# Performance work log

Hardware: AMD Instinct MI355X
Metric: run time of the kernel (lower is better)

Reference implementation:

```python
import jax, jax.numpy as jnp
import numpy as np

jax.config.update("jax_enable_x64", True)

B, N, M_EQ, D_INEQ = 64, 128, 32, 64
RHO = 1.0
THRES = 1e-5
MAX_ITERS = 5000  # safety cap (original loops until relative objective change <= 1e-5)


def setup_inputs() -> dict:
    key = jax.random.key(0)
    kL, kq, kG, kA, kx0, ks = jax.random.split(key, 6)
    L = jax.random.normal(kL, (B, N, N))
    Q = jnp.einsum('bij,bkj->bik', L, L) / N + jnp.eye(N)  # SPD, well-conditioned
    q = jax.random.normal(kq, (B, N))
    G = jax.random.normal(kG, (B, D_INEQ, N))
    A = jax.random.normal(kA, (B, M_EQ, N))
    x0 = jax.random.normal(kx0, (B, N))
    slack = jax.random.uniform(ks, (B, D_INEQ)) + 0.1
    h = jnp.einsum('bdn,bn->bd', G, x0) + slack  # strictly feasible ineq
    b = jnp.einsum('bmn,bn->bm', A, x0)          # feasible eq
    f32 = jnp.float32
    return {"Q": Q.astype(f32), "q": q.astype(f32), "G": G.astype(f32),
            "h": h.astype(f32), "A": A.astype(f32), "b": b.astype(f32)}


def _alt_diff_batch(Q, q, G, h, A, b):
    """Batched Alt-Diff ADMM QP solve; returns (x [B,n], dx/dq [B,n,n])."""
    Bb, n = q.shape
    d = h.shape[1]
    m = b.shape[1]
    dt = Q.dtype
    AtA = jnp.einsum('bmi,bmj->bij', A, A)
    GtG = jnp.einsum('bdi,bdj->bij', G, G)
    R = -jnp.linalg.inv(Q + RHO * AtA + RHO * GtG)
    ATb = RHO * jnp.einsum('bmn,bm->bn', A, b)
    GTh = RHO * jnp.einsum('bdn,bd->bn', G, h)
    eye = jnp.eye(n, dtype=dt)

    def obj(x):
        return 0.5 * jnp.einsum('bi,bij,bj->b', x, Q, x) + jnp.einsum('bi,bi->b', q, x)

    init = dict(
        xk=jnp.zeros((Bb, n), dt), sk=jnp.zeros((Bb, d), dt),
        lamb=jnp.zeros((Bb, m), dt), nu=jnp.zeros((Bb, d), dt),
        dxk=jnp.zeros((Bb, n, n), dt), dsk=jnp.zeros((Bb, d, n), dt),
        dlamb=jnp.zeros((Bb, m, n), dt), dnu=jnp.zeros((Bb, d, n), dt),
        res_prev=jnp.full((Bb,), 1000.0, dt),   # res = [1000, -100] init
        res_cur=jnp.full((Bb,), -100.0, dt),
        done=jnp.zeros((Bb,), bool),
        it=jnp.zeros((), jnp.int32),
    )

    def cond(s):
        return jnp.logical_and(jnp.any(~s["done"]), s["it"] < MAX_ITERS)

    def body(s):
        xk = jnp.einsum('bij,bj->bi', R,
                        q + jnp.einsum('bmn,bm->bn', A, s["lamb"])
                          + jnp.einsum('bdn,bd->bn', G, s["nu"]) - ATb
                          + RHO * jnp.einsum('bdn,bd->bn', G, s["sk"]) - GTh)
        dxk = jnp.einsum('bij,bjk->bik', R,
                         eye + jnp.einsum('bmn,bmk->bnk', A, s["dlamb"])
                             + jnp.einsum('bdn,bdk->bnk', G, s["dnu"])
                             + RHO * jnp.einsum('bdn,bdk->bnk', G, s["dsk"]))
        Gx = jnp.einsum('bdn,bn->bd', G, xk)
        sk = jax.nn.relu(-(1.0 / RHO) * s["nu"] - (Gx - h))
        sgn = (sk > 0).astype(dt)  # sgn applied to already-relu'd sk, as in source
        dsk = (-1.0 / RHO) * sgn[:, :, None] * (s["dnu"] + RHO * jnp.einsum('bdn,bnk->bdk', G, dxk))
        lamb = s["lamb"] + RHO * (jnp.einsum('bmn,bn->bm', A, xk) - b)
        dlamb = s["dlamb"] + RHO * jnp.einsum('bmn,bnk->bmk', A, dxk)
        nu = s["nu"] + RHO * (Gx + sk - h)
        dnu = s["dnu"] + RHO * (jnp.einsum('bdn,bnk->bdk', G, dxk) + dsk)
        res_new = obj(xk)

        keep = s["done"]

        def sel(old, new):
            mask = keep.reshape((-1,) + (1,) * (new.ndim - 1))
            return jnp.where(mask, old, new)

        res_prev = jnp.where(keep, s["res_prev"], s["res_cur"])
        res_cur = jnp.where(keep, s["res_cur"], res_new)
        done = keep | (jnp.abs((res_cur - res_prev) / res_prev) <= THRES)
        return dict(
            xk=sel(s["xk"], xk), sk=sel(s["sk"], sk),
            lamb=sel(s["lamb"], lamb), nu=sel(s["nu"], nu),
            dxk=sel(s["dxk"], dxk), dsk=sel(s["dsk"], dsk),
            dlamb=sel(s["dlamb"], dlamb), dnu=sel(s["dnu"], dnu),
            res_prev=res_prev, res_cur=res_cur, done=done, it=s["it"] + 1,
        )

    final = jax.lax.while_loop(cond, body, init)
    return final["xk"], final["dxk"]


def reference(Q, q, G, h, A, b):
    out_dtype = q.dtype
    f64 = jnp.float64
    x, _dx = _alt_diff_batch(Q.astype(f64), q.astype(f64), G.astype(f64),
                             h.astype(f64), A.astype(f64), b.astype(f64))
    return x.astype(out_dtype)
```

## Files before the change

### kernel.cpp

```cpp
#include <hip/hip_runtime.h>

#define NN 128
#define ME 32
#define DI 64
#define NZ 96
#define ROWD 130
#define MAXIT 5000

#define OFF_UN 16640
#define ROWB  (OFF_UN)
#define COLB  (OFF_UN + 256)
#define FPLO_F (2*(OFF_UN))
#define FPHI_F (2*(OFF_UN) + 512)
#define TV0L  (OFF_UN + 384)
#define TV0H  (OFF_UN + 512)
#define TV1   (OFF_UN + 576)
#define FLG   (OFF_UN + 608)
#define YBUF  (OFF_UN)
#define KBUF  (OFF_UN + 1536)
#define CPART (OFF_UN + 1024)
#define VP    (OFF_UN + 1280)
#define BASEV (OFF_UN + 1792)
#define QBV   (OFF_UN + 1888)
#define FPART (OFF_UN + 1024)
#define RHSV  (OFF_UN + 1280)
#define XPART (OFF_UN + 1408)
#define CB    (OFF_UN + 2688)
#define QBUF  (OFF_UN + 2816)
#define V1    (OFF_UN + 2944)
#define V2    (OFF_UN + 3072)
#define HB    (OFF_UN + 3200)
#define BB    (OFF_UN + 3264)
#define CST   (OFF_UN + 3296)
#define ZBF   (OFF_UN + 3304)
#define LDS_DBL (OFF_UN + 3400)

typedef __attribute__((ext_vector_type(2))) float f32x2;

__device__ __forceinline__ float rlf(float v, int lane) {
  return __uint_as_float((unsigned)__builtin_amdgcn_readlane((int)__float_as_uint(v), lane));
}
__device__ __forceinline__ f32x2 fma2(f32x2 a, f32x2 b, f32x2 c) {
  return __builtin_elementwise_fma(a, b, c);
}

#define CPYRANGE(LBASE, KBASE, CNT)                                        \
  _Pragma("unroll") for (int j = 0; j < (CNT); ++j) {                      \
    const int lj = (LBASE) + j, kc = (KBASE) + j;                          \
    float va = (float)ldsd[KBUF + kc*NZ + l];                              \
    float vb = (float)ldsd[KBUF + kc*NZ + 64 + lm];                        \
    if ((lj & 1) == 0) { Kp[lj>>1].x = va; Kp2[lj>>1].x = vb; }            \
    else               { Kp[lj>>1].y = va; Kp2[lj>>1].y = vb; }            \
  }

#define MV2(PA, ZS, L0) {                                                  \
    f32x2 z0 = { rlf(ZS, L0), rlf(ZS, (L0)+1) };                           \
    A0 = fma2(Kp[PA], z0, A0); B0 = fma2(Kp2[PA], z0, B0);                 \
    f32x2 z1 = { rlf(ZS, (L0)+2), rlf(ZS, (L0)+3) };                       \
    A1 = fma2(Kp[(PA)+1], z1, A1); B1 = fma2(Kp2[(PA)+1], z1, B1); }
#define MV1(PA, ZS, L0) {                                                  \
    f32x2 z0 = { rlf(ZS, L0), rlf(ZS, (L0)+1) };                           \
    A0 = fma2(Kp[PA], z0, A0); B0 = fma2(Kp2[PA], z0, B0); }

__global__ __launch_bounds__(256, 1) void altdiff_kernel(
    const float* __restrict__ Qg, const float* __restrict__ qg,
    const float* __restrict__ Gg, const float* __restrict__ hg,
    const float* __restrict__ Ag, const float* __restrict__ bg,
    float* __restrict__ out)
{
  extern __shared__ double ldsd[];
  float* const ldsf = (float*)ldsd;

  const int bidx = blockIdx.x;
  const int tid  = threadIdx.x;
  const int w    = tid >> 6;
  const int l    = tid & 63;
  const int lm   = l & 31;
  const int ia   = tid & 127;
  const int hh   = tid >> 7;

  const float* Qb = Qg + (size_t)bidx * NN * NN;
  const float* Ab = Ag + (size_t)bidx * ME * NN;
  const float* Gb = Gg + (size_t)bidx * DI * NN;
  const float* qb = qg + (size_t)bidx * NN;
  const float* hb = hg + (size_t)bidx * DI;
  const float* bv = bg + (size_t)bidx * ME;

  if (tid < DI) ldsd[HB + tid] = (double)hb[tid];
  else if (tid < DI + ME) ldsd[BB + tid - DI] = (double)bv[tid - DI];
  if (tid >= 128) ldsd[QBUF + tid - 128] = (double)qb[tid - 128];

  const int r = tid >> 4, c = tid & 15;
  double acc[8][8];

  {
    const float4* Q4 = (const float4*)Qb;
#pragma unroll
    for (int rr = 0; rr < 8; ++rr) {
      float4 q0 = Q4[((8*r+rr) << 5) + 2*c];
      float4 q1 = Q4[((8*r+rr) << 5) + 2*c + 1];
      acc[rr][0]=(double)q0.x; acc[rr][1]=(double)q0.y; acc[rr][2]=(double)q0.z; acc[rr][3]=(double)q0.w;
      acc[rr][4]=(double)q1.x; acc[rr][5]=(double)q1.y; acc[rr][6]=(double)q1.z; acc[rr][7]=(double)q1.w;
    }
    const float4* A4 = (const float4*)Ab;
    for (int m = 0; m < ME; ++m) {
      float4 u0 = A4[(m << 5) + 2*r], u1 = A4[(m << 5) + 2*r + 1];
      float4 v0 = A4[(m << 5) + 2*c], v1 = A4[(m << 5) + 2*c + 1];
      double uu[8] = {(double)u0.x,(double)u0.y,(double)u0.z,(double)u0.w,
                      (double)u1.x,(double)u1.y,(double)u1.z,(double)u1.w};
      double vv[8] = {(double)v0.x,(double)v0.y,(double)v0.z,(double)v0.w,
                      (double)v1.x,(double)v1.y,(double)v1.z,(double)v1.w};
#pragma unroll
      for (int rr = 0; rr < 8; ++rr)
#pragma unroll
        for (int cc = 0; cc < 8; ++cc)
          acc[rr][cc] = fma(uu[rr], vv[cc], acc[rr][cc]);
    }
    const float4* G4 = (const float4*)Gb;
    for (int d = 0; d < DI; ++d) {
      float4 u0 = G4[(d << 5) + 2*r], u1 = G4[(d << 5) + 2*r + 1];
      float4 v0 = G4[(d << 5) + 2*c], v1 = G4[(d << 5) + 2*c + 1];
      double uu[8] = {(double)u0.x,(double)u0.y,(double)u0.z,(double)u0.w,
                      (double)u1.x,(double)u1.y,(double)u1.z,(double)u1.w};
      double vv[8] = {(double)v0.x,(double)v0.y,(double)v0.z,(double)v0.w,
                      (double)v1.x,(double)v1.y,(double)v1.z,(double)v1.w};
#pragma unroll
      for (int rr = 0; rr < 8; ++rr)
#pragma unroll
        for (int cc = 0; cc < 8; ++cc)
          acc[rr][cc] = fma(uu[rr], vv[cc], acc[rr][cc]);
    }
  }

  {
    if (r == 0) {
#pragma unroll
      for (int cc = 0; cc < 8; ++cc) ldsd[ROWB + 8*c + cc] = acc[0][cc];
    }
    if (c == 0) {
#pragma unroll
      for (int rr = 0; rr < 8; ++rr) ldsd[COLB + 8*r + rr] = acc[rr][0];
    }
    __syncthreads();
    for (int k = 0; k < NN; ++k) {
      const int pb = (k & 1) << 7;
      const int krt = k >> 3, kcl = k & 7;
      double rowk[8], colv[8];
#pragma unroll
      for (int cc = 0; cc < 8; ++cc) rowk[cc] = ldsd[ROWB + pb + 8*c + cc];
#pragma unroll
      for (int rr = 0; rr < 8; ++rr) colv[rr] = ldsd[COLB + pb + 8*r + rr];
      const double dkk  = ldsd[ROWB + pb + k];
      const double rcpd = 1.0 / dkk;
      double rdv[8];
#pragma unroll
      for (int cc = 0; cc < 8; ++cc) rdv[cc] = rowk[cc] * rcpd;
      const bool pivR = (r == krt), pivC = (c == krt);
#pragma unroll
      for (int rr = 0; rr < 8; ++rr) {
        const double cv = colv[rr] * rcpd;
        const bool pr = pivR && (rr == kcl);
#pragma unroll
        for (int cc = 0; cc < 8; ++cc) {
          double gen = fma(-cv, rowk[cc], acc[rr][cc]);
          acc[rr][cc] = pr ? rdv[cc] : gen;
        }
      }
      if (pivC) {
#pragma unroll
        for (int cc = 0; cc < 8; ++cc) if (cc == kcl) {
#pragma unroll
          for (int rr = 0; rr < 8; ++rr) {
            const bool pr2 = pivR && (rr == kcl);
            acc[rr][cc] = pr2 ? -rcpd : colv[rr] * rcpd;
          }
        }
      }
      if (k < NN - 1) {
        const int pb2 = ((k + 1) & 1) << 7;
        const int krt2 = (k + 1) >> 3, kcl2 = (k + 1) & 7;
        if (r == krt2) {
#pragma unroll
          for (int rr = 0; rr < 8; ++rr) if (rr == kcl2) {
#pragma unroll
            for (int cc = 0; cc < 8; ++cc) ldsd[ROWB + pb2 + 8*c + cc] = acc[rr][cc];
          }
        }
        if (c == krt2) {
#pragma unroll
          for (int cc = 0; cc < 8; ++cc) if (cc == kcl2) {
#pragma unroll
            for (int rr = 0; rr < 8; ++rr) ldsd[COLB + pb2 + 8*r + rr] = acc[rr][cc];
          }
        }
      }
      __syncthreads();
    }
#pragma unroll
    for (int rr = 0; rr < 8; ++rr) {
      double2* dst = (double2*)(ldsd + (8*r+rr)*ROWD + 8*c);
#pragma unroll
      for (int t = 0; t < 4; ++t) dst[t] = make_double2(acc[rr][2*t], acc[rr][2*t+1]);
    }
  }
  __syncthreads();

  f32x2 Kp[15], Kp2[15];
  for (int blk = 0; blk < 8; ++blk) {
    {
      const float* gp[6];
#pragma unroll
      for (int jj = 0; jj < 6; ++jj) {
        int it = 12*blk + 6*hh + jj;
        gp[jj] = (it < DI) ? (Gb + it*NN) : (Ab + (it - DI)*NN);
      }
      double a2[6] = {0,0,0,0,0,0};
#pragma unroll 4
      for (int t = 0; t < NN; ++t) {
        double rv = ldsd[t*ROWD + ia];
#pragma unroll
        for (int jj = 0; jj < 6; ++jj)
          a2[jj] = fma(rv, (double)gp[jj][t], a2[jj]);
      }
      double2* yst = (double2*)(ldsd + YBUF + ia*12 + 6*hh);
#pragma unroll
      for (int p = 0; p < 3; ++p) yst[p] = make_double2(a2[2*p], a2[2*p+1]);
    }
    __syncthreads();
    {
      const int r2 = (ia < NZ) ? ia : 0;
      const float* brow = (r2 < DI) ? (Gb + r2*NN) : (Ab + (r2 - DI)*NN);
      double a2[6] = {0,0,0,0,0,0};
#pragma unroll 4
      for (int t = 0; t < NN; ++t) {
        double bvv = (double)brow[t];
        const double2* yr = (const double2*)(ldsd + YBUF + t*12 + 6*hh);
        double2 y0 = yr[0], y1 = yr[1], y2 = yr[2];
        a2[0] = fma(bvv, y0.x, a2[0]); a2[1] = fma(bvv, y0.y, a2[1]);
        a2[2] = fma(bvv, y1.x, a2[2]); a2[3] = fma(bvv, y1.y, a2[3]);
        a2[4] = fma(bvv, y2.x, a2[4]); a2[5] = fma(bvv, y2.y, a2[5]);
      }
      if (ia < NZ) {
#pragma unroll
        for (int jj = 0; jj < 6; ++jj) ldsd[KBUF + (6*hh + jj)*NZ + ia] = a2[jj];
      }
    }
    __syncthreads();
    if (w == 0) {
      if (blk == 0)      { CPYRANGE(0,  0, 12) }
      else if (blk == 1) { CPYRANGE(12, 0, 12) }
    } else if (w == 1) {
      if (blk == 2)      { CPYRANGE(0,  0, 12) }
      else if (blk == 3) { CPYRANGE(12, 0, 4) }
    } else if (w == 2) {
      if (blk == 3)      { CPYRANGE(0,  4, 8) }
      else if (blk == 4) { CPYRANGE(8,  0, 12) }
      else if (blk == 5) { CPYRANGE(20, 0, 10) }
    } else {
      if (blk == 5)      { CPYRANGE(0,  10, 2) }
      else if (blk == 6) { CPYRANGE(2,  0, 12) }
      else if (blk == 7) { CPYRANGE(14, 0, 12) }
    }
    __syncthreads();
  }

  {
    double s = 0;
#pragma unroll 8
    for (int jc = 0; jc < 48; ++jc) {
      int j = 48*hh + jc;
      double coef = (j < DI) ? ldsd[HB + j] : ldsd[BB + j - DI];
      const float* src = (j < DI) ? (Gb + j*NN) : (Ab + (j - DI)*NN);
      s = fma(-(double)src[ia], coef, s);
    }
    ldsd[CPART + hh*128 + ia] = s;
  }
  __syncthreads();
  if (tid < NN) ldsd[CB + tid] = ldsd[QBUF + tid] + ldsd[CPART + tid] + ldsd[CPART + 128 + tid];
  __syncthreads();

  {
    double a = 0, b2 = 0;
#pragma unroll 4
    for (int tt = 0; tt < 64; ++tt) {
      int t = 64*hh + tt;
      double rv = ldsd[t*ROWD + ia];
      a  = fma(rv, ldsd[CB + t], a);
      b2 = fma(rv, ldsd[QBUF + t], b2);
    }
    ldsd[VP + hh*128 + ia] = a;
    ldsd[VP + 256 + hh*128 + ia] = b2;
  }
  __syncthreads();
  if (tid < NN) {
    ldsd[V1 + tid] = ldsd[VP + tid] + ldsd[VP + 128 + tid];
    ldsd[V2 + tid] = ldsd[VP + 256 + tid] + ldsd[VP + 384 + tid];
  }
  __syncthreads();

  {
    const int r2 = (ia < NZ) ? ia : 0;
    const float* brow = (r2 < DI) ? (Gb + r2*NN) : (Ab + (r2 - DI)*NN);
    const int voff = hh ? V2 : V1;
    double s = 0;
#pragma unroll 4
    for (int t = 0; t < NN; ++t) s = fma((double)brow[t], ldsd[voff + t], s);
    if (ia < NZ) ldsd[(hh ? QBV : BASEV) + ia] = s;
  }
  if (w == 0) {
    double pc = ldsd[V1+l]*ldsd[CB+l]   + ldsd[V1+64+l]*ldsd[CB+64+l];
    double pq = ldsd[V1+l]*ldsd[QBUF+l] + ldsd[V1+64+l]*ldsd[QBUF+64+l];
#pragma unroll
    for (int off = 32; off >= 1; off >>= 1) { pc += __shfl_xor(pc, off); pq += __shfl_xor(pq, off); }
    if (l == 0) { ldsd[CST] = pc; ldsd[CST+1] = pq; }
  }
  __syncthreads();

  const double baseA = ldsd[BASEV + l];
  const double baseB = ldsd[BASEV + 64 + lm];
  const double qvA   = ldsd[QBV + l];
  const double qvB   = ldsd[QBV + 64 + lm];
  const double hb2   = ldsd[HB + l] - baseA;
  const double bb2   = baseB - ldsd[BB + lm];
  const double S_uc  = ldsd[CST], S_qu = ldsd[CST + 1];
  double hnb = hb2, lb = bb2;
  double zlo = 0.0, zhi = 0.0;
  double zAlo = 0.0, zAhi = 0.0, zBlo = 0.0, zBhi = 0.0, zClo = 0.0, zChi = 0.0;
  double res_prev = 1000.0, res_cur = -100.0;

  {
    ldsf[FPLO_F + (w << 6) + l] = 0.f;
    if (l < 32) ldsf[FPHI_F + (w << 5) + l] = 0.f;
    if (tid == 0) { ldsd[FLG] = 0.0; ldsd[FLG + 1] = 0.0; }
  }

  for (int it = 0; it < MAXIT + 3; ++it) {
    __syncthreads();
    const int buf = it & 1, nbuf = buf ^ 1;
    const int bprev = (it + 1) & 1;
    double fl = ldsd[FLG + bprev];
    float p0 = 0.f, p1 = 0.f, p2 = 0.f, p3 = 0.f, q0 = 0.f, q1 = 0.f, q2 = 0.f, q3 = 0.f;
    if (w != 3) {
      const int fb = FPLO_F + (buf << 8) + l;
      p0 = ldsf[fb]; p1 = ldsf[fb + 64]; p2 = ldsf[fb + 128]; p3 = ldsf[fb + 192];
    }
    if (w >= 2) {
      const int fb = FPHI_F + (buf << 7) + lm;
      q0 = ldsf[fb]; q1 = ldsf[fb + 32]; q2 = ldsf[fb + 64]; q3 = ldsf[fb + 96];
    }
    double t1v[16];
    if (w == 1) {
      const double2* tp = (const double2*)(ldsd + TV1 + bprev*16);
#pragma unroll
      for (int u = 0; u < 8; ++u) { double2 v = tp[u]; t1v[2*u] = v.x; t1v[2*u+1] = v.y; }
    }
    double a40 = 0, a41 = 0, a42 = 0, a43 = 0, a44 = 0, a45 = 0;
    if (w == 3) {
      const int g = l & 15;
      const double* tl = ldsd + TV0L + bprev*64;
      const double* th = ldsd + TV0H + bprev*32;
      a40 = tl[g]; a41 = tl[g + 16]; a42 = tl[g + 32]; a43 = tl[g + 48];
      a44 = th[g]; a45 = th[g + 16];
    }
    double slo = 0.0, t = 0.0, shi = 0.0, lamn = 0.0;
    float zflo = 0.f, zfhi = 0.f;
    if (w != 3) {
      float s = (p0 + p1) + (p2 + p3);
      slo = (double)s; t = hnb - slo;
      zflo = (float)fabs(t);
    }
    if (w >= 2) {
      float sh = (q0 + q1) + (q2 + q3);
      shi = (double)sh; lamn = lb + shi;
      zfhi = (float)lamn;
    }
    if (it >= 3 && fl != 0.0) break;
    if (w == 0) { zClo = zBlo; zBlo = zAlo; zAlo = zlo; }
    if (w == 3) { zChi = zBhi; zBhi = zAhi; zAhi = zhi; }
    if (it < MAXIT) {
      if (w == 0) zlo = fabs(t);
      if (w != 3) hnb = hb2 + fmin(t, 0.0);
      if (w == 3) zhi = lamn;
      if (w >= 2) lb = lamn + bb2;
      f32x2 A0 = {0.f, 0.f}, A1 = A0, B0 = A0, B1 = A0;
      if (w == 0) {
        MV2(0, zflo, 0)  MV2(2, zflo, 4)  MV2(4, zflo, 8)
        MV2(6, zflo, 12) MV2(8, zflo, 16) MV2(10, zflo, 20)
      } else if (w == 1) {
        MV2(0, zflo, 24) MV2(2, zflo, 28) MV2(4, zflo, 32) MV2(6, zflo, 36)
      } else if (w == 2) {
        MV2(0, zflo, 40) MV2(2, zflo, 44) MV2(4, zflo, 48)
        MV2(6, zflo, 52) MV2(8, zflo, 56) MV2(10, zflo, 60)
        MV2(12, zfhi, 0) MV1(14, zfhi, 4)
      } else {
        MV2(0, zfhi, 6)  MV2(2, zfhi, 10) MV2(4, zfhi, 14)
        MV2(6, zfhi, 18) MV2(8, zfhi, 22) MV2(10, zfhi, 26)
        MV1(12, zfhi, 30)
      }
      f32x2 As = A0 + A1, Bs = B0 + B1;
      float pa0 = As.x + As.y;
      float pa1 = Bs.x + Bs.y;
      ldsf[FPLO_F + (nbuf << 8) + (w << 6) + l] = pa0;
      if (l < 32) ldsf[FPHI_F + (nbuf << 7) + (w << 5) + l] = pa1;
      if (w == 0) {
        double yfull = slo + baseA;
        double tvl = fma(qvA, zAlo, -0.5*(zAlo*(baseA + yfull) + yfull*yfull));
        ldsd[TV0L + buf*64 + l] = tvl;
      }
      if (w == 3) {
        double yfB = shi + baseB;
        double tvh = fma(qvB, zAhi, -0.5*(zAhi*(baseB + yfB) + yfB*yfB));
        if (l < 32) ldsd[TV0H + buf*32 + l] = tvh;
      }
    }
    if (w == 3 && l < 16 && it >= 1 && it <= MAXIT)
      ldsd[TV1 + buf*16 + l] = ((a40 + a41) + (a42 + a43)) + (a44 + a45);
    if (w == 1 && it >= 2 && it <= MAXIT + 1) {
      double s1 = ((t1v[0] + t1v[1]) + (t1v[2] + t1v[3])) + ((t1v[4] + t1v[5]) + (t1v[6] + t1v[7]));
      double s2 = ((t1v[8] + t1v[9]) + (t1v[10] + t1v[11])) + ((t1v[12] + t1v[13]) + (t1v[14] + t1v[15]));
      double obj = (s1 + s2) - 0.5*S_uc + S_qu;
      res_prev = res_cur; res_cur = obj;
      if (l == 0)
        ldsd[FLG + buf] = (fabs(res_cur - res_prev) <= 1e-5 * fabs(res_prev)) ? 1.0 : 0.0;
    }
  }

  if (w == 0) ldsd[ZBF + l] = zClo;
  if (w == 3 && l < 32) ldsd[ZBF + 64 + l] = zChi;
  __syncthreads();
  {
    double s = 0;
#pragma unroll 8
    for (int jc = 0; jc < 48; ++jc) {
      int j = 48*hh + jc;
      double zj = ldsd[ZBF + j];
      const float* src = (j < DI) ? (Gb + j*NN) : (Ab + (j - DI)*NN);
      s = fma((double)src[ia], zj, s);
    }
    ldsd[FPART + hh*128 + ia] = s;
  }
  __syncthreads();
  if (tid < NN) ldsd[RHSV + tid] = ldsd[CB + tid] + ldsd[FPART + tid] + ldsd[FPART + 128 + tid];
  __syncthreads();
  {
    double s = 0;
#pragma unroll 4
    for (int tt = 0; tt < 64; ++tt) {
      int t = 64*hh + tt;
      s = fma(ldsd[t*ROWD + ia], ldsd[RHSV + t], s);
    }
    ldsd[XPART + hh*128 + ia] = s;
  }
  __syncthreads();
  if (tid < NN)
    out[(size_t)bidx * NN + tid] = (float)(ldsd[XPART + tid] + ldsd[XPART + 128 + tid]);
}

extern "C" void kernel_launch(void* const* d_in, const int* in_sizes, int n_in,
                              void* d_out, int out_size, void* d_ws, size_t ws_size,
                              hipStream_t stream) {
  (void)in_sizes; (void)n_in; (void)out_size; (void)d_ws; (void)ws_size;
  const float* Q = (const float*)d_in[0];
  const float* q = (const float*)d_in[1];
  const float* G = (const float*)d_in[2];
  const float* h = (const float*)d_in[3];
  const float* A = (const float*)d_in[4];
  const float* b = (const float*)d_in[5];
  float* out = (float*)d_out;
  const size_t lds_bytes = (size_t)LDS_DBL * sizeof(double);
  altdiff_kernel<<<dim3(64), dim3(256), lds_bytes, stream>>>(Q, q, G, h, A, b, out);
}
```

Before: 686.0 us.

## Add fifth wavefront for objective tracking and rebalance ADMM matvec across four waves

Launches 320 threads per block. A dedicated fifth wavefront handles objective evaluation, the reduction and the convergence flag, so the four compute waves only run the per-iteration matvec and the projection/dual updates. The K rows are redistributed so each of the four waves owns exactly 24 columns, and the partial-sum buffers are packed as float2. The objective terms now go through LDS exchange buffers, and the prologue/epilogue phases are guarded with tid<256, which adds some sync and occupancy cost.

```diff
diff --git a/kernel.cpp b/kernel.cpp
--- a/kernel.cpp
+++ b/kernel.cpp
@@ -10,12 +10,12 @@
 #define OFF_UN 16640
 #define ROWB  (OFF_UN)
 #define COLB  (OFF_UN + 256)
-#define FPLO_F (2*(OFF_UN))
-#define FPHI_F (2*(OFF_UN) + 512)
-#define TV0L  (OFF_UN + 384)
-#define TV0H  (OFF_UN + 512)
-#define TV1   (OFF_UN + 576)
-#define FLG   (OFF_UN + 608)
+#define PPK   (OFF_UN)
+#define ZEXL  (OFF_UN + 512)
+#define ZEXH  (OFF_UN + 640)
+#define TVX   (OFF_UN + 704)
+#define TV16  (OFF_UN + 832)
+#define FLG   (OFF_UN + 864)
 #define YBUF  (OFF_UN)
 #define KBUF  (OFF_UN + 1536)
 #define CPART (OFF_UN + 1024)
@@ -44,32 +44,19 @@
   return __builtin_elementwise_fma(a, b, c);
 }
 
-#define CPYRANGE(LBASE, KBASE, CNT)                                        \
-  _Pragma("unroll") for (int j = 0; j < (CNT); ++j) {                      \
-    const int lj = (LBASE) + j, kc = (KBASE) + j;                          \
-    float va = (float)ldsd[KBUF + kc*NZ + l];                              \
-    float vb = (float)ldsd[KBUF + kc*NZ + 64 + lm];                        \
-    if ((lj & 1) == 0) { Kp[lj>>1].x = va; Kp2[lj>>1].x = vb; }            \
-    else               { Kp[lj>>1].y = va; Kp2[lj>>1].y = vb; }            \
-  }
-
 #define MV2(PA, ZS, L0) {                                                  \
     f32x2 z0 = { rlf(ZS, L0), rlf(ZS, (L0)+1) };                           \
     A0 = fma2(Kp[PA], z0, A0); B0 = fma2(Kp2[PA], z0, B0);                 \
     f32x2 z1 = { rlf(ZS, (L0)+2), rlf(ZS, (L0)+3) };                       \
     A1 = fma2(Kp[(PA)+1], z1, A1); B1 = fma2(Kp2[(PA)+1], z1, B1); }
-#define MV1(PA, ZS, L0) {                                                  \
-    f32x2 z0 = { rlf(ZS, L0), rlf(ZS, (L0)+1) };                           \
-    A0 = fma2(Kp[PA], z0, A0); B0 = fma2(Kp2[PA], z0, B0); }
-
-__global__ __launch_bounds__(256, 1) void altdiff_kernel(
+
+__global__ __launch_bounds__(320, 1) void altdiff_kernel(
     const float* __restrict__ Qg, const float* __restrict__ qg,
     const float* __restrict__ Gg, const float* __restrict__ hg,
     const float* __restrict__ Ag, const float* __restrict__ bg,
     float* __restrict__ out)
 {
   extern __shared__ double ldsd[];
-  float* const ldsf = (float*)ldsd;
 
   const int bidx = blockIdx.x;
   const int tid  = threadIdx.x;
@@ -88,12 +75,12 @@
 
   if (tid < DI) ldsd[HB + tid] = (double)hb[tid];
   else if (tid < DI + ME) ldsd[BB + tid - DI] = (double)bv[tid - DI];
-  if (tid >= 128) ldsd[QBUF + tid - 128] = (double)qb[tid - 128];
+  if (tid >= 128 && tid < 256) ldsd[QBUF + tid - 128] = (double)qb[tid - 128];
 
   const int r = tid >> 4, c = tid & 15;
   double acc[8][8];
 
-  {
+  if (tid < 256) {
     const float4* Q4 = (const float4*)Qb;
 #pragma unroll
     for (int rr = 0; rr < 8; ++rr) {
@@ -132,7 +119,7 @@
     }
   }
 
-  {
+  if (tid < 256) {
     if (r == 0) {
 #pragma unroll
       for (int cc = 0; cc < 8; ++cc) ldsd[ROWB + 8*c + cc] = acc[0][cc];
@@ -141,8 +128,10 @@
 #pragma unroll
       for (int rr = 0; rr < 8; ++rr) ldsd[COLB + 8*r + rr] = acc[rr][0];
     }
-    __syncthreads();
-    for (int k = 0; k < NN; ++k) {
+  }
+  __syncthreads();
+  for (int k = 0; k < NN; ++k) {
+    if (tid < 256) {
       const int pb = (k & 1) << 7;
       const int krt = k >> 3, kcl = k & 7;
       double rowk[8], colv[8];
@@ -194,8 +183,10 @@
           }
         }
       }
-      __syncthreads();
-    }
+    }
+    __syncthreads();
+  }
+  if (tid < 256) {
 #pragma unroll
     for (int rr = 0; rr < 8; ++rr) {
       double2* dst = (double2*)(ldsd + (8*r+rr)*ROWD + 8*c);
@@ -205,9 +196,9 @@
   }
   __syncthreads();
 
-  f32x2 Kp[15], Kp2[15];
+  f32x2 Kp[12], Kp2[12];
   for (int blk = 0; blk < 8; ++blk) {
-    {
+    if (tid < 256) {
       const float* gp[6];
 #pragma unroll
       for (int jj = 0; jj < 6; ++jj) {
@@ -227,7 +218,7 @@
       for (int p = 0; p < 3; ++p) yst[p] = make_double2(a2[2*p], a2[2*p+1]);
     }
     __syncthreads();
-    {
+    if (tid < 256) {
       const int r2 = (ia < NZ) ? ia : 0;
       const float* brow = (r2 < DI) ? (Gb + r2*NN) : (Ab + (r2 - DI)*NN);
       double a2[6] = {0,0,0,0,0,0};
@@ -246,25 +237,29 @@
       }
     }
     __syncthreads();
-    if (w == 0) {
-      if (blk == 0)      { CPYRANGE(0,  0, 12) }
-      else if (blk == 1) { CPYRANGE(12, 0, 12) }
-    } else if (w == 1) {
-      if (blk == 2)      { CPYRANGE(0,  0, 12) }
-      else if (blk == 3) { CPYRANGE(12, 0, 4) }
-    } else if (w == 2) {
-      if (blk == 3)      { CPYRANGE(0,  4, 8) }
-      else if (blk == 4) { CPYRANGE(8,  0, 12) }
-      else if (blk == 5) { CPYRANGE(20, 0, 10) }
-    } else {
-      if (blk == 5)      { CPYRANGE(0,  10, 2) }
-      else if (blk == 6) { CPYRANGE(2,  0, 12) }
-      else if (blk == 7) { CPYRANGE(14, 0, 12) }
+    if (w == (blk >> 1)) {
+      if ((blk & 1) == 0) {
+#pragma unroll
+        for (int p = 0; p < 6; ++p) {
+          Kp [p].x = (float)ldsd[KBUF + (2*p  )*NZ + l];
+          Kp [p].y = (float)ldsd[KBUF + (2*p+1)*NZ + l];
+          Kp2[p].x = (float)ldsd[KBUF + (2*p  )*NZ + 64 + lm];
+          Kp2[p].y = (float)ldsd[KBUF + (2*p+1)*NZ + 64 + lm];
+        }
+      } else {
+#pragma unroll
+        for (int p = 0; p < 6; ++p) {
+          Kp [6+p].x = (float)ldsd[KBUF + (2*p  )*NZ + l];
+          Kp [6+p].y = (float)ldsd[KBUF + (2*p+1)*NZ + l];
+          Kp2[6+p].x = (float)ldsd[KBUF + (2*p  )*NZ + 64 + lm];
+          Kp2[6+p].y = (float)ldsd[KBUF + (2*p+1)*NZ + 64 + lm];
+        }
+      }
     }
     __syncthreads();
   }
 
-  {
+  if (tid < 256) {
     double s = 0;
 #pragma unroll 8
     for (int jc = 0; jc < 48; ++jc) {
@@ -279,7 +274,7 @@
   if (tid < NN) ldsd[CB + tid] = ldsd[QBUF + tid] + ldsd[CPART + tid] + ldsd[CPART + 128 + tid];
   __syncthreads();
 
-  {
+  if (tid < 256) {
     double a = 0, b2 = 0;
 #pragma unroll 4
     for (int tt = 0; tt < 64; ++tt) {
@@ -298,7 +293,7 @@
   }
   __syncthreads();
 
-  {
+  if (tid < 256) {
     const int r2 = (ia < NZ) ? ia : 0;
     const float* brow = (r2 < DI) ? (Gb + r2*NN) : (Ab + (r2 - DI)*NN);
     const int voff = hh ? V2 : V1;
@@ -329,106 +324,98 @@
   double res_prev = 1000.0, res_cur = -100.0;
 
   {
-    ldsf[FPLO_F + (w << 6) + l] = 0.f;
-    if (l < 32) ldsf[FPHI_F + (w << 5) + l] = 0.f;
+    if (w < 4) ((float2*)&ldsd[PPK + (w << 6) + l])[0] = make_float2(0.f, 0.f);
+    if (w == 0) ldsd[ZEXL + 64 + l] = 0.0;
+    if (w == 3 && l < 32) ldsd[ZEXH + 32 + l] = 0.0;
     if (tid == 0) { ldsd[FLG] = 0.0; ldsd[FLG + 1] = 0.0; }
   }
 
   for (int it = 0; it < MAXIT + 3; ++it) {
     __syncthreads();
     const int buf = it & 1, nbuf = buf ^ 1;
-    const int bprev = (it + 1) & 1;
-    double fl = ldsd[FLG + bprev];
-    float p0 = 0.f, p1 = 0.f, p2 = 0.f, p3 = 0.f, q0 = 0.f, q1 = 0.f, q2 = 0.f, q3 = 0.f;
-    if (w != 3) {
-      const int fb = FPLO_F + (buf << 8) + l;
-      p0 = ldsf[fb]; p1 = ldsf[fb + 64]; p2 = ldsf[fb + 128]; p3 = ldsf[fb + 192];
-    }
-    if (w >= 2) {
-      const int fb = FPHI_F + (buf << 7) + lm;
-      q0 = ldsf[fb]; q1 = ldsf[fb + 32]; q2 = ldsf[fb + 64]; q3 = ldsf[fb + 96];
-    }
-    double t1v[16];
-    if (w == 1) {
-      const double2* tp = (const double2*)(ldsd + TV1 + bprev*16);
-#pragma unroll
-      for (int u = 0; u < 8; ++u) { double2 v = tp[u]; t1v[2*u] = v.x; t1v[2*u+1] = v.y; }
-    }
-    double a40 = 0, a41 = 0, a42 = 0, a43 = 0, a44 = 0, a45 = 0;
-    if (w == 3) {
+    const int bprev = nbuf;
+    const double fl = ldsd[FLG + bprev];
+
+    if (w < 4) {
+      const float2* pb = (const float2*)(ldsd + PPK + buf*256);
+      float2 v0 = pb[l], v1 = pb[64 + l], v2 = pb[128 + l], v3 = pb[192 + l];
+      double t = 0.0, lamn = 0.0;
+      float zflo = 0.f, zfhi = 0.f;
+      if (w != 3) {
+        float s = (v0.x + v1.x) + (v2.x + v3.x);
+        t = hnb - (double)s;
+        zflo = (float)fabs(t);
+      }
+      if (w >= 2) {
+        float sh = (v0.y + v1.y) + (v2.y + v3.y);
+        lamn = lb + (double)sh;
+        zfhi = (float)lamn;
+      }
+      if (it >= 3 && fl != 0.0) break;
+      if (w == 0) { zClo = zBlo; zBlo = zAlo; zAlo = zlo; }
+      if (w == 3) { zChi = zBhi; zBhi = zAhi; zAhi = zhi; }
+      if (it < MAXIT) {
+        if (w == 0) { zlo = fabs(t); ldsd[ZEXL + buf*64 + l] = zlo; }
+        if (w != 3) hnb = hb2 + fmin(t, 0.0);
+        if (w == 3) { zhi = lamn; if (l < 32) ldsd[ZEXH + buf*32 + l] = lamn; }
+        if (w >= 2) lb = lamn + bb2;
+        f32x2 A0 = {0.f, 0.f}, A1 = A0, B0 = A0, B1 = A0;
+        if (w == 0) {
+          MV2(0, zflo, 0)  MV2(2, zflo, 4)  MV2(4, zflo, 8)
+          MV2(6, zflo, 12) MV2(8, zflo, 16) MV2(10, zflo, 20)
+        } else if (w == 1) {
+          MV2(0, zflo, 24) MV2(2, zflo, 28) MV2(4, zflo, 32)
+          MV2(6, zflo, 36) MV2(8, zflo, 40) MV2(10, zflo, 44)
+        } else if (w == 2) {
+          MV2(0, zflo, 48) MV2(2, zflo, 52) MV2(4, zflo, 56) MV2(6, zflo, 60)
+          MV2(8, zfhi, 0)  MV2(10, zfhi, 4)
+        } else {
+          MV2(0, zfhi, 8)  MV2(2, zfhi, 12) MV2(4, zfhi, 16)
+          MV2(6, zfhi, 20) MV2(8, zfhi, 24) MV2(10, zfhi, 28)
+        }
+        f32x2 As = A0 + A1, Bs = B0 + B1;
+        ((float2*)&ldsd[PPK + nbuf*256 + (w << 6) + l])[0] =
+            make_float2(As.x + As.y, Bs.x + Bs.y);
+      }
+    } else {
+      const float2* pb = (const float2*)(ldsd + PPK + buf*256);
+      float2 v0 = pb[l], v1 = pb[64 + l], v2 = pb[128 + l], v3 = pb[192 + l];
+      const double zAl = ldsd[ZEXL + bprev*64 + l];
+      const double zAh = ldsd[ZEXH + bprev*32 + lm];
       const int g = l & 15;
-      const double* tl = ldsd + TV0L + bprev*64;
-      const double* th = ldsd + TV0H + bprev*32;
-      a40 = tl[g]; a41 = tl[g + 16]; a42 = tl[g + 32]; a43 = tl[g + 48];
-      a44 = th[g]; a45 = th[g + 16];
-    }
-    double slo = 0.0, t = 0.0, shi = 0.0, lamn = 0.0;
-    float zflo = 0.f, zfhi = 0.f;
-    if (w != 3) {
-      float s = (p0 + p1) + (p2 + p3);
-      slo = (double)s; t = hnb - slo;
-      zflo = (float)fabs(t);
-    }
-    if (w >= 2) {
-      float sh = (q0 + q1) + (q2 + q3);
-      shi = (double)sh; lamn = lb + shi;
-      zfhi = (float)lamn;
-    }
-    if (it >= 3 && fl != 0.0) break;
-    if (w == 0) { zClo = zBlo; zBlo = zAlo; zAlo = zlo; }
-    if (w == 3) { zChi = zBhi; zBhi = zAhi; zAhi = zhi; }
-    if (it < MAXIT) {
-      if (w == 0) zlo = fabs(t);
-      if (w != 3) hnb = hb2 + fmin(t, 0.0);
-      if (w == 3) zhi = lamn;
-      if (w >= 2) lb = lamn + bb2;
-      f32x2 A0 = {0.f, 0.f}, A1 = A0, B0 = A0, B1 = A0;
-      if (w == 0) {
-        MV2(0, zflo, 0)  MV2(2, zflo, 4)  MV2(4, zflo, 8)
-        MV2(6, zflo, 12) MV2(8, zflo, 16) MV2(10, zflo, 20)
-      } else if (w == 1) {
-        MV2(0, zflo, 24) MV2(2, zflo, 28) MV2(4, zflo, 32) MV2(6, zflo, 36)
-      } else if (w == 2) {
-        MV2(0, zflo, 40) MV2(2, zflo, 44) MV2(4, zflo, 48)
-        MV2(6, zflo, 52) MV2(8, zflo, 56) MV2(10, zflo, 60)
-        MV2(12, zfhi, 0) MV1(14, zfhi, 4)
-      } else {
-        MV2(0, zfhi, 6)  MV2(2, zfhi, 10) MV2(4, zfhi, 14)
-        MV2(6, zfhi, 18) MV2(8, zfhi, 22) MV2(10, zfhi, 26)
-        MV1(12, zfhi, 30)
-      }
-      f32x2 As = A0 + A1, Bs = B0 + B1;
-      float pa0 = As.x + As.y;
-      float pa1 = Bs.x + Bs.y;
-      ldsf[FPLO_F + (nbuf << 8) + (w << 6) + l] = pa0;
-      if (l < 32) ldsf[FPHI_F + (nbuf << 7) + (w << 5) + l] = pa1;
-      if (w == 0) {
-        double yfull = slo + baseA;
-        double tvl = fma(qvA, zAlo, -0.5*(zAlo*(baseA + yfull) + yfull*yfull));
-        ldsd[TV0L + buf*64 + l] = tvl;
-      }
-      if (w == 3) {
-        double yfB = shi + baseB;
-        double tvh = fma(qvB, zAhi, -0.5*(zAhi*(baseB + yfB) + yfB*yfB));
-        if (l < 32) ldsd[TV0H + buf*32 + l] = tvh;
-      }
-    }
-    if (w == 3 && l < 16 && it >= 1 && it <= MAXIT)
-      ldsd[TV1 + buf*16 + l] = ((a40 + a41) + (a42 + a43)) + (a44 + a45);
-    if (w == 1 && it >= 2 && it <= MAXIT + 1) {
-      double s1 = ((t1v[0] + t1v[1]) + (t1v[2] + t1v[3])) + ((t1v[4] + t1v[5]) + (t1v[6] + t1v[7]));
-      double s2 = ((t1v[8] + t1v[9]) + (t1v[10] + t1v[11])) + ((t1v[12] + t1v[13]) + (t1v[14] + t1v[15]));
-      double obj = (s1 + s2) - 0.5*S_uc + S_qu;
-      res_prev = res_cur; res_cur = obj;
-      if (l == 0)
-        ldsd[FLG + buf] = (fabs(res_cur - res_prev) <= 1e-5 * fabs(res_prev)) ? 1.0 : 0.0;
+      const double* tq = ldsd + TVX + bprev*64;
+      double a0 = tq[g], a1 = tq[g + 16], a2 = tq[g + 32], a3 = tq[g + 48];
+      double t1v[16];
+      const double2* tp = (const double2*)(ldsd + TV16 + bprev*16);
+#pragma unroll
+      for (int u = 0; u < 8; ++u) { double2 vv = tp[u]; t1v[2*u] = vv.x; t1v[2*u+1] = vv.y; }
+      if (it >= 3 && fl != 0.0) break;
+      if (it < MAXIT) {
+        float slo_f = (v0.x + v1.x) + (v2.x + v3.x);
+        float shi_f = (v0.y + v1.y) + (v2.y + v3.y);
+        double yf  = (double)slo_f + baseA;
+        double tvl = fma(qvA, zAl, -0.5*(zAl*(baseA + yf) + yf*yf));
+        double yfB = (double)shi_f + baseB;
+        double tvh = fma(qvB, zAh, -0.5*(zAh*(baseB + yfB) + yfB*yfB));
+        ldsd[TVX + buf*64 + l] = tvl + ((l < 32) ? tvh : 0.0);
+      }
+      if (l < 16 && it >= 1 && it <= MAXIT)
+        ldsd[TV16 + buf*16 + l] = (a0 + a1) + (a2 + a3);
+      if (it >= 2 && it <= MAXIT + 1) {
+        double s1 = ((t1v[0] + t1v[1]) + (t1v[2] + t1v[3])) + ((t1v[4] + t1v[5]) + (t1v[6] + t1v[7]));
+        double s2 = ((t1v[8] + t1v[9]) + (t1v[10] + t1v[11])) + ((t1v[12] + t1v[13]) + (t1v[14] + t1v[15]));
+        double obj = (s1 + s2) - 0.5*S_uc + S_qu;
+        res_prev = res_cur; res_cur = obj;
+        if (l == 0)
+          ldsd[FLG + buf] = (fabs(res_cur - res_prev) <= 1e-5 * fabs(res_prev)) ? 1.0 : 0.0;
+      }
     }
   }
 
   if (w == 0) ldsd[ZBF + l] = zClo;
   if (w == 3 && l < 32) ldsd[ZBF + 64 + l] = zChi;
   __syncthreads();
-  {
+  if (tid < 256) {
     double s = 0;
 #pragma unroll 8
     for (int jc = 0; jc < 48; ++jc) {
@@ -442,7 +429,7 @@
   __syncthreads();
   if (tid < NN) ldsd[RHSV + tid] = ldsd[CB + tid] + ldsd[FPART + tid] + ldsd[FPART + 128 + tid];
   __syncthreads();
-  {
+  if (tid < 256) {
     double s = 0;
 #pragma unroll 4
     for (int tt = 0; tt < 64; ++tt) {
@@ -468,5 +455,5 @@
   const float* b = (const float*)d_in[5];
   float* out = (float*)d_out;
   const size_t lds_bytes = (size_t)LDS_DBL * sizeof(double);
-  altdiff_kernel<<<dim3(64), dim3(256), lds_bytes, stream>>>(Q, q, G, h, A, b, out);
+  altdiff_kernel<<<dim3(64), dim3(320), lds_bytes, stream>>>(Q, q, G, h, A, b, out);
 }
```

Result: slower. 706.9 us (+3.0%).
